# Optimization experiments

Hardware: AMD Instinct MI355X
Metric: run time of the kernel (lower is better)

Reference implementation:

```python
import jax, jax.numpy as jnp
import numpy as np

QLEN, MLEN, B, DM, H, D, NROLL = 512, 512, 8, 1024, 16, 64, 3
KLEN = QLEN + MLEN
SCALE = 1.0 / float(np.sqrt(D))
EPS = 1e-5


def setup_inputs() -> dict:
    key = jax.random.key(0)
    ks = jax.random.split(key, 5)
    h = jax.random.normal(ks[0], (QLEN, B, DM), jnp.float32)
    mems = jax.random.normal(ks[1], (MLEN, B, DM), jnp.float32)
    Wq = jax.random.normal(ks[2], (H * D, DM), jnp.float32) * 0.02
    Wkv = jax.random.normal(ks[3], (2 * H * D, DM), jnp.float32) * 0.02
    Wo = jax.random.normal(ks[4], (DM, H * D), jnp.float32) * 0.02
    ln_gamma = jnp.ones((DM,), jnp.float32)
    ln_beta = jnp.zeros((DM,), jnp.float32)
    # Transformer-XL causal mask over [mems ; h]: query i may attend keys j <= i + MLEN
    attn_mask = jnp.triu(jnp.ones((QLEN, KLEN), dtype=bool), k=1 + MLEN)
    return dict(h=h, mems=mems, Wq=Wq, Wkv=Wkv, Wo=Wo,
                ln_gamma=ln_gamma, ln_beta=ln_beta, attn_mask=attn_mask)


def _dpfp(x):
    # concat(relu(x), relu(-x)) then multiplicative roll expansion (n_roll copies)
    x = jnp.concatenate([jax.nn.relu(x), jax.nn.relu(-x)], axis=-1)  # [..., 2D]
    return jnp.concatenate([x * jnp.roll(x, i, axis=-1) for i in range(1, NROLL + 1)],
                           axis=-1)  # [..., 2*D*NROLL]


def reference(h, mems, Wq, Wkv, Wo, ln_gamma, ln_beta, attn_mask):
    qlen, bsz = h.shape[0], h.shape[1]
    c = jnp.concatenate([mems, h], axis=0)                      # [klen, B, DM]
    klen = c.shape[0]
    q = (h @ Wq.T).reshape(qlen, bsz, H, D)                     # [i, b, n, d]
    k, v = jnp.split(c @ Wkv.T, 2, axis=-1)
    k = k.reshape(klen, bsz, H, D)
    v = v.reshape(klen, bsz, H, D)
    qf = _dpfp(q)                                               # [i, b, n, 2*D*NROLL]
    kf = _dpfp(k)
    score = jnp.einsum('ibnd,jbnd->ijbn', qf, kf) * SCALE        # [i, j, b, n]
    score = jnp.where(attn_mask[:, :, None, None], 0.0, score)
    denom = jnp.sum(score, axis=1, keepdims=True) + EPS
    prob = score / denom
    attn_vec = jnp.einsum('ijbn,jbnd->ibnd', prob, v).reshape(qlen, bsz, H * D)
    attn_out = attn_vec @ Wo.T
    # post-LN residual (pre_lnorm=False)
    x = h + attn_out
    mu = jnp.mean(x, axis=-1, keepdims=True)
    var = jnp.var(x, axis=-1, keepdims=True)
    return (x - mu) / jnp.sqrt(var + EPS) * ln_gamma + ln_beta
```

## Files before the change

kernel.cpp:

```cpp
#include <hip/hip_runtime.h>

#define QLEN 512
#define MLEN 512
#define KLEN 1024
#define BB   8
#define DMODEL 1024
#define NH   16
#define HD   64
#define NF   384
#define ATT_SCALE 0.125f
#define EPSV 1e-5f

typedef float v4f __attribute__((ext_vector_type(4)));
typedef float f32x16 __attribute__((ext_vector_type(16)));
typedef short bf16x8 __attribute__((ext_vector_type(8)));
typedef long lx2 __attribute__((ext_vector_type(2)));
typedef unsigned int u32x4 __attribute__((ext_vector_type(4)));
typedef unsigned int u32x2 __attribute__((ext_vector_type(2)));
typedef unsigned short u16x8 __attribute__((ext_vector_type(8)));

__device__ __forceinline__ unsigned short f2bf(float f) {
    unsigned int x = __builtin_bit_cast(unsigned int, f);
    x += 0x7fffu + ((x >> 16) & 1u);
    return (unsigned short)(x >> 16);
}

__device__ __forceinline__ void gll16(const void* g, void* l) {
    __builtin_amdgcn_global_load_lds(
        (const __attribute__((address_space(1))) unsigned int*)g,
        (__attribute__((address_space(3))) unsigned int*)l, 16, 0, 0);
}


__global__ __launch_bounds__(256)
void cvt_kernel(const float* __restrict__ h, const float* __restrict__ mems,
                const float* __restrict__ Wkv, const float* __restrict__ Wq,
                const float* __restrict__ Wo,
                unsigned char* __restrict__ c8, unsigned char* __restrict__ wkv8,
                unsigned char* __restrict__ wq8, unsigned short* __restrict__ wob)
{
    int blk = blockIdx.x;
    if (blk >= 5632) {
        int i = ((blk - 5632) * 256 + threadIdx.x) * 4;
        v4f v = *(const v4f*)(Wo + i);
        unsigned int p0, p1;
        asm("v_cvt_pk_bf16_f32 %0, %1, %2" : "=v"(p0) : "v"(v[0]), "v"(v[1]));
        asm("v_cvt_pk_bf16_f32 %0, %1, %2" : "=v"(p1) : "v"(v[2]), "v"(v[3]));
        uint2 u; u.x = p0; u.y = p1;
        *(uint2*)(wob + i) = u;
        return;
    }
    int tid = blk * 256 + threadIdx.x;
    const float* src; unsigned char* dstrow; float scale; int row, k0;
    if (tid < 1048576) {
        int base = tid * 8; row = base >> 10; k0 = base & 1023;
        src = (row < 4096) ? (mems + (size_t)row * 1024)
                           : (h + (size_t)(row - 4096) * 1024);
        dstrow = c8 + (size_t)row * 1024; scale = 1.f;
    } else if (tid < 1310720) {
        int t2 = tid - 1048576; int base = t2 * 8; row = base >> 10; k0 = base & 1023;
        src = Wkv + (size_t)row * 1024; dstrow = wkv8 + (size_t)row * 1024; scale = 32.f;
    } else {
        int t2 = tid - 1310720; int base = t2 * 8; row = base >> 10; k0 = base & 1023;
        src = Wq + (size_t)row * 1024; dstrow = wq8 + (size_t)row * 1024; scale = 32.f;
    }
    v4f a = *(const v4f*)(src + k0);
    v4f b = *(const v4f*)(src + k0 + 4);
    int v0 = __builtin_amdgcn_cvt_pk_fp8_f32(a[0]*scale, a[1]*scale, 0, false);
    v0     = __builtin_amdgcn_cvt_pk_fp8_f32(a[2]*scale, a[3]*scale, v0, true);
    int v1 = __builtin_amdgcn_cvt_pk_fp8_f32(b[0]*scale, b[1]*scale, 0, false);
    v1     = __builtin_amdgcn_cvt_pk_fp8_f32(b[2]*scale, b[3]*scale, v1, true);
    int kk = (k0 & 127) >> 5;
    int lg = (k0 & 31) >> 3;
    uint2 st; st.x = (unsigned int)v0; st.y = (unsigned int)v1;
    *(uint2*)(dstrow + (k0 & ~127) + (lg * 2 + (kk >> 1)) * 16 + (kk & 1) * 8) = st;
}

__global__ __launch_bounds__(256)
void mmfp8_kernel(const unsigned char* __restrict__ c8,
                  const unsigned char* __restrict__ wkv8,
                  const unsigned char* __restrict__ wq8,
                  unsigned short* __restrict__ kraw,
                  unsigned short* __restrict__ vraw,
                  unsigned short* __restrict__ qraw)
{
    __shared__ unsigned char As[128 * 128];
    __shared__ unsigned char Bs[128 * 128];

    const int bid = blockIdx.x;
    const unsigned char *A8, *B8;
    unsigned short *outK, *outV;
    int m0, n0;
    if (bid < 1024) {
        int o = bid & 7, j = bid >> 3;
        m0 = (o * 8 + (j & 7)) * 128;
        n0 = (j >> 3) * 128;
        A8 = c8; B8 = wkv8; outK = kraw; outV = vraw;
    } else {
        int d2 = bid - 1024;
        int o = d2 & 7, j = d2 >> 3;
        m0 = (o * 4 + (j & 3)) * 128;
        n0 = (j >> 2) * 128;
        A8 = c8 + 4194304; B8 = wq8; outK = qraw; outV = nullptr;
    }

    const int t  = threadIdx.x;
    const int w  = t >> 6;
    const int l  = t & 63;
    const int lj = l & 15;
    const int lg = l >> 4;
    const int wr = w >> 1, wc = w & 1;

    const int lrow8 = l >> 3;
    const int gsw   = (l & 7) ^ lrow8;

    v4f acc[4][4] = {};

    for (int s = 0; s < 8; ++s) {
        __syncthreads();
        #pragma unroll
        for (int u = 0; u < 4; ++u) {
            int i  = w * 4 + u;
            int so = (i * 8 + lrow8) * 1024 + s * 128 + gsw * 16;
            gll16(A8 + (size_t)m0 * 1024 + so, (char*)As + i * 1024);
            gll16(B8 + (size_t)n0 * 1024 + so, (char*)Bs + i * 1024);
        }
        __syncthreads();

        lx2 a2[4][2], b2[4][2];
        #pragma unroll
        for (int m = 0; m < 4; ++m) {
            int row = wr * 64 + m * 16 + lj;
            #pragma unroll
            for (int gp = 0; gp < 2; ++gp) {
                int gr = lg * 2 + gp;
                a2[m][gp] = *(const lx2*)(As + row * 128 + ((gr ^ (row & 7)) * 16));
            }
        }
        #pragma unroll
        for (int nn = 0; nn < 4; ++nn) {
            int row = wc * 64 + nn * 16 + lj;
            #pragma unroll
            for (int gp = 0; gp < 2; ++gp) {
                int gr = lg * 2 + gp;
                b2[nn][gp] = *(const lx2*)(Bs + row * 128 + ((gr ^ (row & 7)) * 16));
            }
        }
        __builtin_amdgcn_s_setprio(1);
        #pragma unroll
        for (int kk = 0; kk < 4; ++kk) {
            #pragma unroll
            for (int m = 0; m < 4; ++m)
                #pragma unroll
                for (int nn = 0; nn < 4; ++nn)
                    acc[m][nn] = __builtin_amdgcn_mfma_f32_16x16x32_fp8_fp8(
                                     a2[m][kk >> 1][kk & 1], b2[nn][kk >> 1][kk & 1],
                                     acc[m][nn], 0, 0, 0);
        }
        __builtin_amdgcn_s_setprio(0);
    }

    #pragma unroll
    for (int m = 0; m < 4; ++m) {
        #pragma unroll
        for (int rr = 0; rr < 4; ++rr) {
            int row = m0 + wr * 64 + m * 16 + 4 * lg + rr;
            #pragma unroll
            for (int nn = 0; nn < 4; ++nn) {
                int col = n0 + wc * 64 + nn * 16 + lj;
                float v = acc[m][nn][rr] * 0.03125f;
                if (n0 < 1024) outK[(size_t)row * 1024 + col] = f2bf(v);
                else           outV[(size_t)row * 1024 + (col - 1024)] = f2bf(v);
            }
        }
    }
}

__global__ __launch_bounds__(256)
void mm128_kernel(const unsigned short* __restrict__ Abf,
                  const unsigned short* __restrict__ Bbf,
                  const float* __restrict__ hres,
                  float* __restrict__ xo)
{
    __shared__ unsigned short As[128 * 64];
    __shared__ unsigned short Bs[128 * 64];

    const int t  = threadIdx.x;
    const int w  = t >> 6;
    const int l  = t & 63;
    const int lj = l & 15;
    const int lg = l >> 4;
    const int m0 = blockIdx.x * 128;
    const int n0 = blockIdx.y * 128;
    const int wr = w >> 1, wc = w & 1;
    const int rsub = l >> 3;
    const int csw  = ((l & 7) ^ rsub) * 16;

    v4f acc[4][4] = {};

    for (int s = 0; s < 16; ++s) {
        const int k0b = s * 128;
        __syncthreads();
        #pragma unroll
        for (int u = 0; u < 4; ++u) {
            int ra = w * 32 + u * 8;
            gll16((const char*)Abf + (size_t)(m0 + ra + rsub) * 2048 + k0b + csw,
                  (char*)As + ra * 128);
            gll16((const char*)Bbf + (size_t)(n0 + ra + rsub) * 2048 + k0b + csw,
                  (char*)Bs + ra * 128);
        }
        __syncthreads();
        #pragma unroll
        for (int ks = 0; ks < 2; ++ks) {
            bf16x8 af[4], bfr[4];
            #pragma unroll
            for (int m = 0; m < 4; ++m) {
                int row = wr * 64 + m * 16 + lj;
                int c = ks * 4 + lg;
                af[m] = *(const bf16x8*)((const char*)As + row * 128 +
                                         ((c ^ (row & 7)) * 16));
            }
            #pragma unroll
            for (int nn = 0; nn < 4; ++nn) {
                int row = wc * 64 + nn * 16 + lj;
                int c = ks * 4 + lg;
                bfr[nn] = *(const bf16x8*)((const char*)Bs + row * 128 +
                                           ((c ^ (row & 7)) * 16));
            }
            #pragma unroll
            for (int m = 0; m < 4; ++m)
                #pragma unroll
                for (int nn = 0; nn < 4; ++nn)
                    acc[m][nn] = __builtin_amdgcn_mfma_f32_16x16x32_bf16(
                                     af[m], bfr[nn], acc[m][nn], 0, 0, 0);
        }
    }

    #pragma unroll
    for (int m = 0; m < 4; ++m) {
        #pragma unroll
        for (int rr = 0; rr < 4; ++rr) {
            int row = m0 + wr * 64 + m * 16 + 4 * lg + rr;
            #pragma unroll
            for (int nn = 0; nn < 4; ++nn) {
                int col = n0 + wc * 64 + nn * 16 + lj;
                xo[(size_t)row * 1024 + col] =
                    acc[m][nn][rr] + hres[(size_t)row * 1024 + col];
            }
        }
    }
}

__device__ __forceinline__ float gld(const unsigned short* gr, int idx) {
    return __builtin_bit_cast(float, ((unsigned int)gr[idx]) << 16);
}

template<int FBASE>
__device__ __forceinline__ void dpfp_half8(const unsigned short* __restrict__ gr,
                                           unsigned char* __restrict__ drow)
{
    #pragma unroll
    for (int c = 0; c < 12; ++c) {
        unsigned int w4[4];
        #pragma unroll
        for (int q4 = 0; q4 < 4; ++q4) {
            float p[4];
            #pragma unroll
            for (int e = 0; e < 4; ++e) {
                const int f  = FBASE + c * 16 + q4 * 4 + e;
                const int r  = (f >> 7) + 1;
                const int tt = f & 127;
                const int uu = (tt - r) & 127;
                p[e] = gld(gr, tt) * gld(gr, uu);
            }
            int v = __builtin_amdgcn_cvt_pk_fp8_f32(p[0], p[1], 0, false);
            v     = __builtin_amdgcn_cvt_pk_fp8_f32(p[2], p[3], v, true);
            w4[q4] = (unsigned int)v;
        }
        u32x4 st = {w4[0], w4[1], w4[2], w4[3]};
        *(u32x4*)(drow + c * 1024) = st;
    }
}

__global__ __launch_bounds__(256)
void feat_kernel(const unsigned short* __restrict__ qraw,
                 const unsigned short* __restrict__ kraw,
                 const unsigned short* __restrict__ vraw,
                 unsigned char* __restrict__ qf, unsigned char* __restrict__ kf,
                 unsigned short* __restrict__ vt)
{
    __shared__ __align__(16) char smem[36864];
    const int t   = threadIdx.x;
    const int blk = blockIdx.x;

    if (blk >= 1536) {
        unsigned short (*S)[72] = (unsigned short(*)[72])smem;
        int v = blk - 1536;
        int jc = v & 3, hh = (v >> 2) & 15, b = v >> 6;
        const unsigned short* src = vraw + (size_t)((jc * 256 + t) * 8 + b) * 1024 + hh * 64;
        #pragma unroll
        for (int c = 0; c < 8; ++c)
            *(u32x4*)&S[t][c * 8] = *(const u32x4*)(src + c * 8);
        __syncthreads();
        const int d = t >> 2, qq = t & 3;
        unsigned short* dst = vt + ((size_t)(b * NH + hh) * HD + d) * KLEN + jc * 256 + qq * 64;
        #pragma unroll
        for (int c8 = 0; c8 < 8; ++c8) {
            u16x8 o;
            #pragma unroll
            for (int e = 0; e < 8; ++e) o[e] = S[qq * 64 + c8 * 8 + e][d];
            *(u16x8*)(dst + c8 * 8) = o;
        }
        return;
    }

    unsigned short* G = (unsigned short*)smem;
    const unsigned short* src; unsigned char* dst; int b, hh, seq0;
    if (blk < 512) {
        int bh = blk >> 2, ig = blk & 3;
        b = bh >> 4; hh = bh & 15; seq0 = ig * 128;
        src = qraw; dst = qf + (size_t)bh * 196608;
    } else {
        int blk2 = blk - 512;
        int bh = blk2 >> 3, jg = blk2 & 7;
        b = bh >> 4; hh = bh & 15; seq0 = jg * 128;
        src = kraw; dst = kf + (size_t)bh * 393216;
    }

    #pragma unroll
    for (int p = 0; p < 4; ++p) {
        int u   = p * 256 + t;
        int row = u >> 3;
        int c0  = (u & 7) * 8;
        u32x4 x = *(const u32x4*)(src + ((size_t)(seq0 + row) * 8 + b) * 1024 +
                                  hh * 64 + c0);
        char* gbase = (char*)G + row * 276 + c0 * 2;
        #pragma unroll
        for (int k = 0; k < 4; ++k) {
            unsigned int xk = x[k];
            float x0 = __builtin_bit_cast(float, xk << 16);
            float x1 = __builtin_bit_cast(float, xk & 0xffff0000u);
            float a0 = fmaxf(x0, 0.f), a1 = fmaxf(x1, 0.f);
            float b0 = fmaxf(-x0, 0.f), b1 = fmaxf(-x1, 0.f);
            unsigned int lo, hig;
            asm("v_cvt_pk_bf16_f32 %0, %1, %2" : "=v"(lo) : "v"(a0), "v"(a1));
            asm("v_cvt_pk_bf16_f32 %0, %1, %2" : "=v"(hig) : "v"(b0), "v"(b1));
            *(unsigned int*)(gbase + k * 4)       = lo;
            *(unsigned int*)(gbase + 128 + k * 4) = hig;
        }
    }
    __syncthreads();

    const int w    = t >> 6;
    const int l    = t & 63;
    const int rowc = (w >> 1) * 64 + l;
    const int hs   = w & 1;
    const unsigned short* gr = G + rowc * 138;
    const int seq = seq0 + rowc;
    unsigned char* drow = dst + (size_t)(seq >> 6) * 24576 + (seq & 63) * 16 +
                          hs * 12288;
    if (hs == 0) dpfp_half8<0>(gr, drow);
    else         dpfp_half8<192>(gr, drow);
}

__global__ __launch_bounds__(256, 2)
void attn_mfma_kernel(const unsigned char* __restrict__ qf,
                      const unsigned char* __restrict__ kf,
                      const unsigned short* __restrict__ vt,
                      unsigned short* __restrict__ avec)
{
    __shared__ unsigned char Ks[64 * 384];
    __shared__ unsigned short Vs[64 * 64];
    __shared__ float Ds[4][32];

    const int t  = threadIdx.x;
    const int w  = t >> 6;
    const int l  = t & 63;
    const int li = l & 31;
    const int hi = l >> 5;

    const int bid = blockIdx.x;
    const int it  = (bid >> 3) & 3;
    const int P   = ((bid >> 5) << 3) + (bid & 7);
    const int n   = P & 15;
    const int b   = P >> 4;

    const unsigned char* qpan = qf + (size_t)P * 196608;
    const unsigned char* kpan = kf + (size_t)P * 393216;
    const char* vpan = (const char*)(vt + (size_t)P * HD * KLEN);

    int voff[2];
    #pragma unroll
    for (int uu = 0; uu < 2; ++uu) {
        int s  = (w * 2 + uu) * 64 + l;
        int d  = s >> 3;
        int cl = s & 7;
        int cg = cl ^ (d & 7);
        voff[uu] = d * (KLEN * 2) + cg * 16;
    }

    long qfr[24];
    {
        const unsigned char* qb = qpan + (size_t)(it * 2 + (w >> 1)) * 24576 +
                                  ((w & 1) * 32 + li) * 16 + hi * 8;
        #pragma unroll
        for (int ks = 0; ks < 24; ++ks)
            qfr[ks] = *(const long*)(qb + ks * 1024);
    }

    f32x16 num[2] = {};
    float den_acc = 0.f;

    const int ig         = it * 128 + w * 32 + li;
    const int my_jt_end  = 2 * it + 8 + (w >> 1);
    const int jt_blk_end = 2 * it + 9;

    for (int jt = 0; jt <= jt_blk_end; ++jt) {
        __syncthreads();
        const unsigned char* ktile = kpan + (size_t)jt * 24576;
        #pragma unroll
        for (int u = 0; u < 6; ++u)
            gll16(ktile + (w * 6 + u) * 1024 + l * 16, Ks + (w * 6 + u) * 1024);
        const char* vtile = vpan + jt * 128;
        #pragma unroll
        for (int uu = 0; uu < 2; ++uu)
            gll16(vtile + voff[uu], (char*)Vs + (w * 2 + uu) * 1024);
        __syncthreads();

        if (jt > my_jt_end) continue;

        f32x16 sacc0 = {};
        f32x16 sacc1 = {};
        __builtin_amdgcn_s_setprio(1);
        #pragma unroll
        for (int ks = 0; ks < 24; ++ks) {
            long k0 = *(const long*)(Ks + ks * 1024 + li * 16 + hi * 8);
            long k1 = *(const long*)(Ks + ks * 1024 + (32 + li) * 16 + hi * 8);
            sacc0 = __builtin_amdgcn_mfma_f32_32x32x16_fp8_fp8(k0, qfr[ks], sacc0, 0, 0, 0);
            sacc1 = __builtin_amdgcn_mfma_f32_32x32x16_fp8_fp8(k1, qfr[ks], sacc1, 0, 0, 0);
        }
        __builtin_amdgcn_s_setprio(0);

        if (jt == my_jt_end) {
            const int joff = jt * 64 - MLEN + 4 * hi;
            #pragma unroll
            for (int reg = 0; reg < 16; ++reg) {
                int jr = (reg & 3) + 8 * (reg >> 2);
                if (joff + jr > ig)      sacc0[reg] = 0.f;
                if (joff + 32 + jr > ig) sacc1[reg] = 0.f;
            }
        }
        {
            float dpart = 0.f;
            #pragma unroll
            for (int reg = 0; reg < 16; ++reg) dpart += sacc0[reg] + sacc1[reg];
            den_acc += dpart + __shfl_xor(dpart, 32);
        }

        #pragma unroll
        for (int jf = 0; jf < 2; ++jf) {
            const f32x16 sc = jf ? sacc1 : sacc0;
            unsigned int c01, c23, c45, c67, c89, cab, ccd, cef;
            asm("v_cvt_pk_bf16_f32 %0, %1, %2" : "=v"(c01) : "v"(sc[0]),  "v"(sc[1]));
            asm("v_cvt_pk_bf16_f32 %0, %1, %2" : "=v"(c23) : "v"(sc[2]),  "v"(sc[3]));
            asm("v_cvt_pk_bf16_f32 %0, %1, %2" : "=v"(c45) : "v"(sc[4]),  "v"(sc[5]));
            asm("v_cvt_pk_bf16_f32 %0, %1, %2" : "=v"(c67) : "v"(sc[6]),  "v"(sc[7]));
            asm("v_cvt_pk_bf16_f32 %0, %1, %2" : "=v"(c89) : "v"(sc[8]),  "v"(sc[9]));
            asm("v_cvt_pk_bf16_f32 %0, %1, %2" : "=v"(cab) : "v"(sc[10]), "v"(sc[11]));
            asm("v_cvt_pk_bf16_f32 %0, %1, %2" : "=v"(ccd) : "v"(sc[12]), "v"(sc[13]));
            asm("v_cvt_pk_bf16_f32 %0, %1, %2" : "=v"(cef) : "v"(sc[14]), "v"(sc[15]));
            u32x2 r0 = __builtin_amdgcn_permlane32_swap(c01, c45, false, false);
            u32x2 r1 = __builtin_amdgcn_permlane32_swap(c23, c67, false, false);
            u32x2 r2 = __builtin_amdgcn_permlane32_swap(c89, ccd, false, false);
            u32x2 r3 = __builtin_amdgcn_permlane32_swap(cab, cef, false, false);
            u32x4 pw0 = {r0.x, r1.x, r0.y, r1.y};
            u32x4 pw1 = {r2.x, r3.x, r2.y, r3.y};
            bf16x8 pa0 = __builtin_bit_cast(bf16x8, pw0);
            bf16x8 pa1 = __builtin_bit_cast(bf16x8, pw1);
            __builtin_amdgcn_s_setprio(1);
            #pragma unroll
            for (int dd = 0; dd < 2; ++dd) {
                int d = dd * 32 + li;
                {
                    int cs = (jf * 4 + hi) ^ (d & 7);
                    bf16x8 vb = *(const bf16x8*)((const char*)Vs + d * 128 + cs * 16);
                    num[dd] = __builtin_amdgcn_mfma_f32_32x32x16_bf16(pa0, vb, num[dd], 0, 0, 0);
                }
                {
                    int cs = (jf * 4 + 2 + hi) ^ (d & 7);
                    bf16x8 vb = *(const bf16x8*)((const char*)Vs + d * 128 + cs * 16);
                    num[dd] = __builtin_amdgcn_mfma_f32_32x32x16_bf16(pa1, vb, num[dd], 0, 0, 0);
                }
            }
            __builtin_amdgcn_s_setprio(0);
        }
    }

    if (l < 32) Ds[w][l] = den_acc;
    #pragma unroll
    for (int reg = 0; reg < 16; ++reg) {
        int i_loc = (reg & 3) + 8 * (reg >> 2) + 4 * hi;
        float dv = Ds[w][i_loc];
        float minv = ATT_SCALE / (dv * ATT_SCALE + EPSV);
        int ig2 = it * 128 + w * 32 + i_loc;
        unsigned short* orow = avec + ((size_t)ig2 * BB + b) * DMODEL + n * HD;
        orow[li]      = f2bf(num[0][reg] * minv);
        orow[32 + li] = f2bf(num[1][reg] * minv);
    }
}

__global__ __launch_bounds__(256)
void ln_kernel(const float* __restrict__ x, const float* __restrict__ gamma,
               const float* __restrict__ beta, float* __restrict__ out)
{
    const int row = blockIdx.x;
    const int t = threadIdx.x;
    const float* xr = x + (size_t)row * DMODEL;
    v4f xv = *(const v4f*)(xr + (t << 2));
    float s1 = xv[0] + xv[1] + xv[2] + xv[3];
    float s2 = xv[0]*xv[0] + xv[1]*xv[1] + xv[2]*xv[2] + xv[3]*xv[3];
    #pragma unroll
    for (int off = 32; off > 0; off >>= 1) {
        s1 += __shfl_down(s1, off);
        s2 += __shfl_down(s2, off);
    }
    __shared__ float red[2][4];
    __shared__ float mv[2];
    const int wave = t >> 6;
    if ((t & 63) == 0) { red[0][wave] = s1; red[1][wave] = s2; }
    __syncthreads();
    if (t == 0) {
        float a = red[0][0] + red[0][1] + red[0][2] + red[0][3];
        float q = red[1][0] + red[1][1] + red[1][2] + red[1][3];
        float mu  = a * (1.f / DMODEL);
        float var = q * (1.f / DMODEL) - mu * mu;
        mv[0] = mu;
        mv[1] = rsqrtf(var + EPSV);
    }
    __syncthreads();
    float mu = mv[0], rs = mv[1];
    v4f gv = *(const v4f*)(gamma + (t << 2));
    v4f bv = *(const v4f*)(beta + (t << 2));
    v4f o;
    #pragma unroll
    for (int e = 0; e < 4; ++e) o[e] = (xv[e] - mu) * rs * gv[e] + bv[e];
    *(v4f*)(out + (size_t)row * DMODEL + (t << 2)) = o;
}

extern "C" void kernel_launch(void* const* d_in, const int* in_sizes, int n_in,
                              void* d_out, int out_size, void* d_ws, size_t ws_size,
                              hipStream_t stream)
{
    const float* h     = (const float*)d_in[0];
    const float* mems  = (const float*)d_in[1];
    const float* Wq    = (const float*)d_in[2];
    const float* Wkv   = (const float*)d_in[3];
    const float* Wo    = (const float*)d_in[4];
    const float* gamma = (const float*)d_in[5];
    const float* beta  = (const float*)d_in[6];

    char* ws = (char*)d_ws;
    unsigned char* qf    = (unsigned char*)(ws);
    unsigned char* kf    = (unsigned char*)(ws + 25165824);
    unsigned char* c8    = (unsigned char*)(ws + 75497472);
    unsigned char* wkv8  = (unsigned char*)(ws + 83886080);
    unsigned char* wq8   = (unsigned char*)(ws + 85983232);
    unsigned short* vt   = (unsigned short*)(ws + 92274688);
    unsigned short* kraw = (unsigned short*)(ws + 150994944);
    unsigned short* vraw = (unsigned short*)(ws + 167772160);
    unsigned short* qraw = (unsigned short*)(ws + 184549376);
    unsigned short* avec = qraw;
    float* xws = (float*)(ws);

    unsigned short* wob = (unsigned short*)d_out;

    cvt_kernel<<<6656, 256, 0, stream>>>(h, mems, Wkv, Wq, Wo, c8, wkv8, wq8, wob);
    mmfp8_kernel<<<1280, 256, 0, stream>>>(c8, wkv8, wq8, kraw, vraw, qraw);
    feat_kernel<<<2048, 256, 0, stream>>>(qraw, kraw, vraw, qf, kf, vt);
    attn_mfma_kernel<<<512, 256, 0, stream>>>(qf, kf, vt, avec);
    mm128_kernel<<<dim3(32, 8), 256, 0, stream>>>(avec, wob, h, xws);
    ln_kernel<<<4096, 256, 0, stream>>>(xws, gamma, beta, (float*)d_out);
}
```

Measured before the change: 148.4 us.

## Use two waves per attention block, each computing 64 query rows

The attention kernel now runs 2 waves of 128 threads instead of 4, and each wave handles two 32-row query fragments (A and B). Every K fragment read from LDS is reused by two MFMAs, and every V fragment by two accumulators. This halves LDS fragment traffic per MFMA and gives each wave more independent MFMA chains. In exchange the kernel needs roughly double the registers per wave (launch bounds 128,1), has fewer waves per CU to hide latency, and each thread issues more of the tile loads.

Result: slower. 164.7 us (+11.0%).

```diff
diff --git a/kernel.cpp b/kernel.cpp
--- a/kernel.cpp
+++ b/kernel.cpp
@@ -363,7 +363,28 @@
     else         dpfp_half8<192>(gr, drow);
 }
 
-__global__ __launch_bounds__(256, 2)
+__device__ __forceinline__ void pack_p(const f32x16 sc, bf16x8& pa0, bf16x8& pa1)
+{
+    unsigned int c01, c23, c45, c67, c89, cab, ccd, cef;
+    asm("v_cvt_pk_bf16_f32 %0, %1, %2" : "=v"(c01) : "v"(sc[0]),  "v"(sc[1]));
+    asm("v_cvt_pk_bf16_f32 %0, %1, %2" : "=v"(c23) : "v"(sc[2]),  "v"(sc[3]));
+    asm("v_cvt_pk_bf16_f32 %0, %1, %2" : "=v"(c45) : "v"(sc[4]),  "v"(sc[5]));
+    asm("v_cvt_pk_bf16_f32 %0, %1, %2" : "=v"(c67) : "v"(sc[6]),  "v"(sc[7]));
+    asm("v_cvt_pk_bf16_f32 %0, %1, %2" : "=v"(c89) : "v"(sc[8]),  "v"(sc[9]));
+    asm("v_cvt_pk_bf16_f32 %0, %1, %2" : "=v"(cab) : "v"(sc[10]), "v"(sc[11]));
+    asm("v_cvt_pk_bf16_f32 %0, %1, %2" : "=v"(ccd) : "v"(sc[12]), "v"(sc[13]));
+    asm("v_cvt_pk_bf16_f32 %0, %1, %2" : "=v"(cef) : "v"(sc[14]), "v"(sc[15]));
+    u32x2 r0 = __builtin_amdgcn_permlane32_swap(c01, c45, false, false);
+    u32x2 r1 = __builtin_amdgcn_permlane32_swap(c23, c67, false, false);
+    u32x2 r2 = __builtin_amdgcn_permlane32_swap(c89, ccd, false, false);
+    u32x2 r3 = __builtin_amdgcn_permlane32_swap(cab, cef, false, false);
+    u32x4 pw0 = {r0.x, r1.x, r0.y, r1.y};
+    u32x4 pw1 = {r2.x, r3.x, r2.y, r3.y};
+    pa0 = __builtin_bit_cast(bf16x8, pw0);
+    pa1 = __builtin_bit_cast(bf16x8, pw1);
+}
+
+__global__ __launch_bounds__(128, 1)
 void attn_mfma_kernel(const unsigned char* __restrict__ qf,
                       const unsigned char* __restrict__ kf,
                       const unsigned short* __restrict__ vt,
@@ -371,7 +392,7 @@
 {
     __shared__ unsigned char Ks[64 * 384];
     __shared__ unsigned short Vs[64 * 64];
-    __shared__ float Ds[4][32];
+    __shared__ float Ds[2][2][32];
 
     const int t  = threadIdx.x;
     const int w  = t >> 6;
@@ -380,8 +401,8 @@
     const int hi = l >> 5;
 
     const int bid = blockIdx.x;
+    const int P   = ((bid >> 5) << 3) + (bid & 7);
     const int it  = (bid >> 3) & 3;
-    const int P   = ((bid >> 5) << 3) + (bid & 7);
     const int n   = P & 15;
     const int b   = P >> 4;
 
@@ -389,94 +410,81 @@
     const unsigned char* kpan = kf + (size_t)P * 393216;
     const char* vpan = (const char*)(vt + (size_t)P * HD * KLEN);
 
-    int voff[2];
-    #pragma unroll
-    for (int uu = 0; uu < 2; ++uu) {
-        int s  = (w * 2 + uu) * 64 + l;
+    int voff[4];
+    #pragma unroll
+    for (int uu = 0; uu < 4; ++uu) {
+        int s  = (w * 4 + uu) * 64 + l;
         int d  = s >> 3;
         int cl = s & 7;
         int cg = cl ^ (d & 7);
         voff[uu] = d * (KLEN * 2) + cg * 16;
     }
 
-    long qfr[24];
+    long qfrA[24], qfrB[24];
     {
-        const unsigned char* qb = qpan + (size_t)(it * 2 + (w >> 1)) * 24576 +
-                                  ((w & 1) * 32 + li) * 16 + hi * 8;
-        #pragma unroll
-        for (int ks = 0; ks < 24; ++ks)
-            qfr[ks] = *(const long*)(qb + ks * 1024);
-    }
-
-    f32x16 num[2] = {};
-    float den_acc = 0.f;
-
-    const int ig         = it * 128 + w * 32 + li;
-    const int my_jt_end  = 2 * it + 8 + (w >> 1);
-    const int jt_blk_end = 2 * it + 9;
+        const unsigned char* qb = qpan + (size_t)(it * 2 + w) * 24576 + li * 16 + hi * 8;
+        #pragma unroll
+        for (int ks = 0; ks < 24; ++ks) {
+            qfrA[ks] = *(const long*)(qb + ks * 1024);
+            qfrB[ks] = *(const long*)(qb + ks * 1024 + 512);
+        }
+    }
+
+    f32x16 numA[2] = {}, numB[2] = {};
+    float denA = 0.f, denB = 0.f;
+
+    const int igA        = it * 128 + w * 64 + li;
+    const int my_jt_end  = it * 2 + w + 8;
+    const int jt_blk_end = it * 2 + 9;
 
     for (int jt = 0; jt <= jt_blk_end; ++jt) {
         __syncthreads();
         const unsigned char* ktile = kpan + (size_t)jt * 24576;
         #pragma unroll
-        for (int u = 0; u < 6; ++u)
-            gll16(ktile + (w * 6 + u) * 1024 + l * 16, Ks + (w * 6 + u) * 1024);
+        for (int u = 0; u < 12; ++u)
+            gll16(ktile + (w * 12 + u) * 1024 + l * 16, Ks + (w * 12 + u) * 1024);
         const char* vtile = vpan + jt * 128;
         #pragma unroll
-        for (int uu = 0; uu < 2; ++uu)
-            gll16(vtile + voff[uu], (char*)Vs + (w * 2 + uu) * 1024);
+        for (int uu = 0; uu < 4; ++uu)
+            gll16(vtile + voff[uu], (char*)Vs + (w * 4 + uu) * 1024);
         __syncthreads();
 
         if (jt > my_jt_end) continue;
-
-        f32x16 sacc0 = {};
-        f32x16 sacc1 = {};
-        __builtin_amdgcn_s_setprio(1);
-        #pragma unroll
-        for (int ks = 0; ks < 24; ++ks) {
-            long k0 = *(const long*)(Ks + ks * 1024 + li * 16 + hi * 8);
-            long k1 = *(const long*)(Ks + ks * 1024 + (32 + li) * 16 + hi * 8);
-            sacc0 = __builtin_amdgcn_mfma_f32_32x32x16_fp8_fp8(k0, qfr[ks], sacc0, 0, 0, 0);
-            sacc1 = __builtin_amdgcn_mfma_f32_32x32x16_fp8_fp8(k1, qfr[ks], sacc1, 0, 0, 0);
-        }
-        __builtin_amdgcn_s_setprio(0);
-
-        if (jt == my_jt_end) {
-            const int joff = jt * 64 - MLEN + 4 * hi;
-            #pragma unroll
-            for (int reg = 0; reg < 16; ++reg) {
-                int jr = (reg & 3) + 8 * (reg >> 2);
-                if (joff + jr > ig)      sacc0[reg] = 0.f;
-                if (joff + 32 + jr > ig) sacc1[reg] = 0.f;
-            }
-        }
-        {
-            float dpart = 0.f;
-            #pragma unroll
-            for (int reg = 0; reg < 16; ++reg) dpart += sacc0[reg] + sacc1[reg];
-            den_acc += dpart + __shfl_xor(dpart, 32);
-        }
+        const bool diag = (jt == my_jt_end);
 
         #pragma unroll
         for (int jf = 0; jf < 2; ++jf) {
-            const f32x16 sc = jf ? sacc1 : sacc0;
-            unsigned int c01, c23, c45, c67, c89, cab, ccd, cef;
-            asm("v_cvt_pk_bf16_f32 %0, %1, %2" : "=v"(c01) : "v"(sc[0]),  "v"(sc[1]));
-            asm("v_cvt_pk_bf16_f32 %0, %1, %2" : "=v"(c23) : "v"(sc[2]),  "v"(sc[3]));
-            asm("v_cvt_pk_bf16_f32 %0, %1, %2" : "=v"(c45) : "v"(sc[4]),  "v"(sc[5]));
-            asm("v_cvt_pk_bf16_f32 %0, %1, %2" : "=v"(c67) : "v"(sc[6]),  "v"(sc[7]));
-            asm("v_cvt_pk_bf16_f32 %0, %1, %2" : "=v"(c89) : "v"(sc[8]),  "v"(sc[9]));
-            asm("v_cvt_pk_bf16_f32 %0, %1, %2" : "=v"(cab) : "v"(sc[10]), "v"(sc[11]));
-            asm("v_cvt_pk_bf16_f32 %0, %1, %2" : "=v"(ccd) : "v"(sc[12]), "v"(sc[13]));
-            asm("v_cvt_pk_bf16_f32 %0, %1, %2" : "=v"(cef) : "v"(sc[14]), "v"(sc[15]));
-            u32x2 r0 = __builtin_amdgcn_permlane32_swap(c01, c45, false, false);
-            u32x2 r1 = __builtin_amdgcn_permlane32_swap(c23, c67, false, false);
-            u32x2 r2 = __builtin_amdgcn_permlane32_swap(c89, ccd, false, false);
-            u32x2 r3 = __builtin_amdgcn_permlane32_swap(cab, cef, false, false);
-            u32x4 pw0 = {r0.x, r1.x, r0.y, r1.y};
-            u32x4 pw1 = {r2.x, r3.x, r2.y, r3.y};
-            bf16x8 pa0 = __builtin_bit_cast(bf16x8, pw0);
-            bf16x8 pa1 = __builtin_bit_cast(bf16x8, pw1);
+            f32x16 sA = {}, sB = {};
+            __builtin_amdgcn_s_setprio(1);
+            #pragma unroll
+            for (int ks = 0; ks < 24; ++ks) {
+                long kk = *(const long*)(Ks + ks * 1024 + (jf * 32 + li) * 16 + hi * 8);
+                sA = __builtin_amdgcn_mfma_f32_32x32x16_fp8_fp8(kk, qfrA[ks], sA, 0, 0, 0);
+                sB = __builtin_amdgcn_mfma_f32_32x32x16_fp8_fp8(kk, qfrB[ks], sB, 0, 0, 0);
+            }
+            __builtin_amdgcn_s_setprio(0);
+
+            if (diag) {
+                const int joff = jt * 64 - MLEN + jf * 32 + 4 * hi;
+                #pragma unroll
+                for (int reg = 0; reg < 16; ++reg) {
+                    int jr = (reg & 3) + 8 * (reg >> 2);
+                    if (joff + jr > igA)      sA[reg] = 0.f;
+                    if (joff + jr > igA + 32) sB[reg] = 0.f;
+                }
+            }
+            {
+                float dA = 0.f, dB = 0.f;
+                #pragma unroll
+                for (int reg = 0; reg < 16; ++reg) { dA += sA[reg]; dB += sB[reg]; }
+                denA += dA + __shfl_xor(dA, 32);
+                denB += dB + __shfl_xor(dB, 32);
+            }
+
+            bf16x8 pa0A, pa1A, pa0B, pa1B;
+            pack_p(sA, pa0A, pa1A);
+            pack_p(sB, pa0B, pa1B);
+
             __builtin_amdgcn_s_setprio(1);
             #pragma unroll
             for (int dd = 0; dd < 2; ++dd) {
@@ -484,28 +492,33 @@
                 {
                     int cs = (jf * 4 + hi) ^ (d & 7);
                     bf16x8 vb = *(const bf16x8*)((const char*)Vs + d * 128 + cs * 16);
-                    num[dd] = __builtin_amdgcn_mfma_f32_32x32x16_bf16(pa0, vb, num[dd], 0, 0, 0);
+                    numA[dd] = __builtin_amdgcn_mfma_f32_32x32x16_bf16(pa0A, vb, numA[dd], 0, 0, 0);
+                    numB[dd] = __builtin_amdgcn_mfma_f32_32x32x16_bf16(pa0B, vb, numB[dd], 0, 0, 0);
                 }
                 {
                     int cs = (jf * 4 + 2 + hi) ^ (d & 7);
                     bf16x8 vb = *(const bf16x8*)((const char*)Vs + d * 128 + cs * 16);
-                    num[dd] = __builtin_amdgcn_mfma_f32_32x32x16_bf16(pa1, vb, num[dd], 0, 0, 0);
+                    numA[dd] = __builtin_amdgcn_mfma_f32_32x32x16_bf16(pa1A, vb, numA[dd], 0, 0, 0);
+                    numB[dd] = __builtin_amdgcn_mfma_f32_32x32x16_bf16(pa1B, vb, numB[dd], 0, 0, 0);
                 }
             }
             __builtin_amdgcn_s_setprio(0);
         }
     }
 
-    if (l < 32) Ds[w][l] = den_acc;
+    if (l < 32) { Ds[w][0][l] = denA; Ds[w][1][l] = denB; }
     #pragma unroll
     for (int reg = 0; reg < 16; ++reg) {
         int i_loc = (reg & 3) + 8 * (reg >> 2) + 4 * hi;
-        float dv = Ds[w][i_loc];
-        float minv = ATT_SCALE / (dv * ATT_SCALE + EPSV);
-        int ig2 = it * 128 + w * 32 + i_loc;
-        unsigned short* orow = avec + ((size_t)ig2 * BB + b) * DMODEL + n * HD;
-        orow[li]      = f2bf(num[0][reg] * minv);
-        orow[32 + li] = f2bf(num[1][reg] * minv);
+        float mA = ATT_SCALE / (Ds[w][0][i_loc] * ATT_SCALE + EPSV);
+        float mB = ATT_SCALE / (Ds[w][1][i_loc] * ATT_SCALE + EPSV);
+        int giA = it * 128 + w * 64 + i_loc;
+        unsigned short* orA = avec + ((size_t)giA * BB + b) * DMODEL + n * HD;
+        unsigned short* orB = avec + ((size_t)(giA + 32) * BB + b) * DMODEL + n * HD;
+        orA[li]      = f2bf(numA[0][reg] * mA);
+        orA[32 + li] = f2bf(numA[1][reg] * mA);
+        orB[li]      = f2bf(numB[0][reg] * mB);
+        orB[32 + li] = f2bf(numB[1][reg] * mB);
     }
 }
 
@@ -577,7 +590,7 @@
     cvt_kernel<<<6656, 256, 0, stream>>>(h, mems, Wkv, Wq, Wo, c8, wkv8, wq8, wob);
     mmfp8_kernel<<<1280, 256, 0, stream>>>(c8, wkv8, wq8, kraw, vraw, qraw);
     feat_kernel<<<2048, 256, 0, stream>>>(qraw, kraw, vraw, qf, kf, vt);
-    attn_mfma_kernel<<<512, 256, 0, stream>>>(qf, kf, vt, avec);
+    attn_mfma_kernel<<<512, 128, 0, stream>>>(qf, kf, vt, avec);
     mm128_kernel<<<dim3(32, 8), 256, 0, stream>>>(avec, wob, h, xws);
     ln_kernel<<<4096, 256, 0, stream>>>(xws, gamma, beta, (float*)d_out);
 }
```
